# Kernel tuning notes

Hardware: AMD Instinct MI355X
Metric: run time of the kernel (lower is better)

## Reference

```python
import jax, jax.numpy as jnp
import numpy as np

B, T, H, NH, HD = 2, 2048, 2048, 16, 128


def setup_inputs() -> dict:
    key = jax.random.key(0)
    k1, k2, k3 = jax.random.split(key, 3)
    hidden_states = jax.random.normal(k1, (B, T, H), dtype=jnp.float32)
    w_qkv = jax.random.normal(k2, (3 * H, H), dtype=jnp.float32) * (1.0 / np.sqrt(H))
    w_out = jax.random.normal(k3, (H, H), dtype=jnp.float32) * (1.0 / np.sqrt(H))
    return {"hidden_states": hidden_states, "w_qkv": w_qkv, "w_out": w_out}


def reference(hidden_states, w_qkv, w_out):
    scale = 1.0 / np.sqrt(HD)
    # qkv projection: torch Linear is x @ W.T with W [out, in]
    qkv = jnp.einsum('bth,oh->bto', hidden_states, w_qkv)  # [B, T, 3H]
    q, k, v = jnp.split(qkv, 3, axis=2)
    # [B, NH, T, HD]
    q = q.reshape(B, T, NH, HD).transpose(0, 2, 1, 3)
    k = k.reshape(B, T, NH, HD).transpose(0, 2, 1, 3)
    v = v.reshape(B, T, NH, HD).transpose(0, 2, 1, 3)
    scores = jnp.einsum('bhqd,bhkd->bhqk', q, k) * scale  # [B, NH, T, T]
    mask = jnp.tril(jnp.ones((T, T), dtype=bool))  # causal
    scores = jnp.where(mask[None, None], scores, -jnp.inf)
    probs = jax.nn.softmax(scores, axis=-1)
    attn = jnp.einsum('bhqk,bhkd->bhqd', probs, v)  # [B, NH, T, HD]
    attn = attn.transpose(0, 2, 1, 3).reshape(B, T, H)
    out = jnp.einsum('bth,oh->bto', attn, w_out)
    return out
```

## Files before the change

kernel.cpp:

```cpp
#include <hip/hip_runtime.h>
#include <cstdint>
#include <cstddef>

typedef _Float16 f16x8 __attribute__((ext_vector_type(8)));
typedef _Float16 f16x4 __attribute__((ext_vector_type(4)));
typedef float    f32x4 __attribute__((ext_vector_type(4)));
typedef unsigned short ushort_t;

#define LOG2E 1.4426950408889634f

constexpr int BATCH = 2;
constexpr int TSEQ  = 2048;
constexpr int HID   = 2048;
constexpr int NH    = 16;
constexpr int HD    = 128;
constexpr int GK    = 2048;
constexpr int NKT   = GK / 64;

__device__ inline f32x4 mfma16(f16x8 a, f16x8 b, f32x4 c) {
    return __builtin_amdgcn_mfma_f32_16x16x32_f16(a, b, c, 0, 0, 0);
}

__device__ inline void async_copy16(const void* src, void* dst_lds) {
    __builtin_amdgcn_global_load_lds(
        (const __attribute__((address_space(1))) uint32_t*)src,
        (__attribute__((address_space(3))) uint32_t*)dst_lds, 16, 0, 0);
}

__global__ __launch_bounds__(256)
void cast_f32_f16(const float4* __restrict__ in, f16x4* __restrict__ out, int n4) {
    int i = blockIdx.x * 256 + threadIdx.x;
    if (i >= n4) return;
    float4 v = in[i];
    f16x4 o = { (_Float16)v.x, (_Float16)v.y, (_Float16)v.z, (_Float16)v.w };
    out[i] = o;
}

template <int MODE>
__global__ __launch_bounds__(512, 2)
void gemm_bt(const _Float16* __restrict__ A, const _Float16* __restrict__ B,
             float* __restrict__ C, _Float16* __restrict__ Qo,
             _Float16* __restrict__ Ko, _Float16* __restrict__ Vo, int NB) {
    __shared__ __align__(16) _Float16 As[3][256 * 64];
    __shared__ __align__(16) _Float16 Bs[3][128 * 64];

    const int tid  = threadIdx.x;
    const int lane = tid & 63;
    const int w    = tid >> 6;
    const int l15  = lane & 15;
    const int lq   = lane >> 4;
    const int wr   = w >> 1, wc = w & 1;

    const int bid = (int)blockIdx.x;
    const int cpx = (int)gridDim.x >> 3;
    const int swz = (bid & 7) * cpx + (bid >> 3);
    const int bn  = swz % NB, bm = swz / NB;
    const int m0  = bm * 256, n0 = bn * 128;

    const _Float16* Ab = A + (size_t)m0 * GK;
    const _Float16* Bb = B + (size_t)n0 * GK;

    auto stage = [&](int t, int b) {
        const int k0 = t * 64;
        #pragma unroll
        for (int it = 0; it < 4; ++it) {
            const int slot = it * 512 + tid;
            const int row = slot >> 3, c16 = slot & 7;
            const int srcb = c16 ^ (row & 7);
            async_copy16(Ab + (size_t)row * GK + k0 + srcb * 8,
                         (char*)As[b] + slot * 16);
        }
        #pragma unroll
        for (int it = 0; it < 2; ++it) {
            const int slot = it * 512 + tid;
            const int row = slot >> 3, c16 = slot & 7;
            const int srcb = c16 ^ (row & 7);
            async_copy16(Bb + (size_t)row * GK + k0 + srcb * 8,
                         (char*)Bs[b] + slot * 16);
        }
    };

    f32x4 acc[4][4] = {};

    stage(0, 0);
    stage(1, 1);

    for (int t = 0; t < NKT; ++t) {
        if (t + 1 < NKT) asm volatile("s_waitcnt vmcnt(6)" ::: "memory");
        else             asm volatile("s_waitcnt vmcnt(0)" ::: "memory");
        __builtin_amdgcn_s_barrier();
        __builtin_amdgcn_sched_barrier(0);

        const char* At_ = (const char*)As[t % 3];
        const char* Bt_ = (const char*)Bs[t % 3];

        f16x8 af[4][2], bff[4][2];
        #pragma unroll
        for (int i = 0; i < 4; ++i)
            #pragma unroll
            for (int kk = 0; kk < 2; ++kk) {
                const int ra = wr * 64 + i * 16 + l15;
                af[i][kk]  = *(const f16x8*)(At_ + ra * 128 + (((kk * 4 + lq) ^ (ra & 7)) << 4));
                const int rb = wc * 64 + i * 16 + l15;
                bff[i][kk] = *(const f16x8*)(Bt_ + rb * 128 + (((kk * 4 + lq) ^ (rb & 7)) << 4));
            }

        if (t + 2 < NKT) stage(t + 2, (t + 2) % 3);

        __builtin_amdgcn_s_setprio(1);
        #pragma unroll
        for (int kk = 0; kk < 2; ++kk)
            #pragma unroll
            for (int i = 0; i < 4; ++i)
                #pragma unroll
                for (int j = 0; j < 4; ++j)
                    acc[i][j] = mfma16(af[i][kk], bff[j][kk], acc[i][j]);
        __builtin_amdgcn_s_setprio(0);
    }

    if (MODE == 0) {
        #pragma unroll
        for (int j = 0; j < 4; ++j) {
            const int ncol = n0 + wc * 64 + j * 16 + l15;
            const int which = ncol >> 11;
            const int oo = ncol & 2047;
            const int head = oo >> 7;
            const int d = oo & 127;
            _Float16* dst = (which == 0) ? Qo : (which == 1) ? Ko : Vo;
            const float scl = (which == 0) ? 0.08838834764831845f : 1.0f;
            #pragma unroll
            for (int i = 0; i < 4; ++i) {
                #pragma unroll
                for (int r = 0; r < 4; ++r) {
                    const int m = m0 + wr * 64 + i * 16 + lq * 4 + r;
                    const int b = m >> 11, tt = m & 2047;
                    dst[((size_t)(b * NH + head) * TSEQ + tt) * HD + d] =
                        (_Float16)(acc[i][j][r] * scl);
                }
            }
        }
    } else {
        #pragma unroll
        for (int i = 0; i < 4; ++i)
            #pragma unroll
            for (int j = 0; j < 4; ++j)
                #pragma unroll
                for (int r = 0; r < 4; ++r) {
                    const int m = m0 + wr * 64 + i * 16 + lq * 4 + r;
                    const int n = n0 + wc * 64 + j * 16 + l15;
                    C[(size_t)m * HID + n] = acc[i][j][r];
                }
    }
}

__global__ __launch_bounds__(256)
void attn_fwd(const _Float16* __restrict__ Q, const _Float16* __restrict__ K,
              const _Float16* __restrict__ V, _Float16* __restrict__ O) {
    __shared__ __align__(16) char Ks[2][64 * 256];
    __shared__ __align__(16) char Vt[2][128 * 128];
    __shared__ __align__(16) char Ps[4][2048];

    const int tid  = threadIdx.x;
    const int lane = tid & 63;
    const int w    = tid >> 6;
    const int l15  = lane & 15;
    const int lq   = lane >> 4;

    const int bh   = (int)blockIdx.x & 31;
    const int pair = (int)blockIdx.x >> 5;
    const int b = bh >> 4, h = bh & 15;

    const size_t base = (size_t)bh * TSEQ * HD;
    const _Float16* Qp = Q + base;
    const _Float16* Kp = K + base;
    const _Float16* Vp = V + base;

    const f16x8 ones = { (_Float16)1.f, (_Float16)1.f, (_Float16)1.f, (_Float16)1.f,
                         (_Float16)1.f, (_Float16)1.f, (_Float16)1.f, (_Float16)1.f };

    uint4 vv[4];
    auto loadV = [&](int t) {
        const int row = tid & 63;
        #pragma unroll
        for (int it = 0; it < 4; ++it) {
            const int c8 = w * 4 + it;
            vv[it] = *(const uint4*)(Vp + (size_t)(t * 64 + row) * HD + c8 * 8);
        }
    };
    auto stageK = [&](int t, int buf) {
        #pragma unroll
        for (int it = 0; it < 4; ++it) {
            const int slot = it * 256 + tid;
            const int row = slot >> 4, c16 = slot & 15;
            const int srcb = c16 ^ (row & 7);
            async_copy16(Kp + (size_t)(t * 64 + row) * HD + srcb * 8, Ks[buf] + slot * 16);
        }
    };
    auto writeV = [&](int buf) {
        const int row = tid & 63;
        #pragma unroll
        for (int it = 0; it < 4; ++it) {
            const int c8 = w * 4 + it;
            const uint32_t wrd[4] = {vv[it].x, vv[it].y, vv[it].z, vv[it].w};
            #pragma unroll
            for (int p2 = 0; p2 < 4; ++p2) {
                const int d0 = c8 * 8 + p2 * 2, d1 = d0 + 1;
                int b0 = d0 * 128 + row * 2; b0 ^= (d0 & 7) << 4;
                int b1 = d1 * 128 + row * 2; b1 ^= (d1 & 7) << 4;
                *(ushort_t*)(Vt[buf] + b0) = (ushort_t)(wrd[p2] & 0xffffu);
                *(ushort_t*)(Vt[buf] + b1) = (ushort_t)(wrd[p2] >> 16);
            }
        }
    };

    char* Pb = Ps[w];

    for (int phase = 0; phase < 2; ++phase) {
        const int qt = phase ? pair : (31 - pair);
        const int q0 = qt * 64;
        const int NT = qt + 1;

        if (phase) __syncthreads();

        const int qrow = q0 + w * 16 + l15;
        f16x8 qf[4];
        #pragma unroll
        for (int ks = 0; ks < 4; ++ks)
            qf[ks] = *(const f16x8*)(Qp + (size_t)qrow * HD + ks * 32 + lq * 8);

        f32x4 o[8] = {};
        f32x4 osum = {};
        float m_run[4];
        #pragma unroll
        for (int r = 0; r < 4; ++r) m_run[r] = -1e30f;

        loadV(0);
        stageK(0, 0);

        int cur = 0;
        for (int t = 0; t < NT; ++t) {
            writeV(cur);
            __syncthreads();
            if (t + 1 < NT) {
                loadV(t + 1);
                stageK(t + 1, cur ^ 1);
            }

            const int kv0 = t * 64;
            f32x4 s[4] = {};
            __builtin_amdgcn_s_setprio(1);
            #pragma unroll
            for (int ks = 0; ks < 4; ++ks) {
                #pragma unroll
                for (int nf = 0; nf < 4; ++nf) {
                    const int r   = nf * 16 + l15;
                    const int blk = (ks * 4 + lq) ^ (r & 7);
                    const f16x8 kf = *(const f16x8*)(Ks[cur] + r * 256 + blk * 16);
                    s[nf] = mfma16(qf[ks], kf, s[nf]);
                }
            }
            __builtin_amdgcn_s_setprio(0);

            if (kv0 + 63 > q0 + w * 16) {
                #pragma unroll
                for (int nf = 0; nf < 4; ++nf) {
                    const int kvp = kv0 + nf * 16 + l15;
                    #pragma unroll
                    for (int r = 0; r < 4; ++r)
                        if (kvp > q0 + w * 16 + lq * 4 + r) s[nf][r] = -1e30f;
                }
            }

            bool need = false;
            #pragma unroll
            for (int r = 0; r < 4; ++r) {
                const float v = fmaxf(fmaxf(s[0][r], s[1][r]), fmaxf(s[2][r], s[3][r]));
                need = need || (v > m_run[r] + 5.0f);
            }
            if (__any(need)) {
                float alpha[4];
                #pragma unroll
                for (int r = 0; r < 4; ++r) {
                    float v = fmaxf(fmaxf(s[0][r], s[1][r]), fmaxf(s[2][r], s[3][r]));
                    v = fmaxf(v, __shfl_xor(v, 1));
                    v = fmaxf(v, __shfl_xor(v, 2));
                    v = fmaxf(v, __shfl_xor(v, 4));
                    v = fmaxf(v, __shfl_xor(v, 8));
                    const float mn = fmaxf(m_run[r], v);
                    alpha[r] = __builtin_exp2f((m_run[r] - mn) * LOG2E);
                    m_run[r] = mn;
                }
                #pragma unroll
                for (int df = 0; df < 8; ++df)
                    #pragma unroll
                    for (int r = 0; r < 4; ++r)
                        o[df][r] *= alpha[r];
                #pragma unroll
                for (int r = 0; r < 4; ++r) osum[r] *= alpha[r];
            }

            #pragma unroll
            for (int nf = 0; nf < 4; ++nf) {
                #pragma unroll
                for (int r = 0; r < 4; ++r) {
                    const float p = __builtin_exp2f((s[nf][r] - m_run[r]) * LOG2E);
                    const int qp = lq * 4 + r;
                    int byt = qp * 128 + (nf * 16 + l15) * 2;
                    byt ^= (qp & 7) << 4;
                    union { _Float16 hf; ushort_t u; } cv;
                    cv.hf = (_Float16)p;
                    *(ushort_t*)(Pb + byt) = cv.u;
                }
            }

            __builtin_amdgcn_s_setprio(1);
            #pragma unroll
            for (int ks2 = 0; ks2 < 2; ++ks2) {
                const int pblk = (ks2 * 4 + lq) ^ (l15 & 7);
                const f16x8 pf = *(const f16x8*)(Pb + l15 * 128 + pblk * 16);
                #pragma unroll
                for (int df = 0; df < 8; ++df) {
                    const int vr   = df * 16 + l15;
                    const int vblk = (ks2 * 4 + lq) ^ (vr & 7);
                    const f16x8 vf = *(const f16x8*)(Vt[cur] + vr * 128 + vblk * 16);
                    o[df] = mfma16(pf, vf, o[df]);
                }
                osum = mfma16(pf, ones, osum);
            }
            __builtin_amdgcn_s_setprio(0);
            cur ^= 1;
        }

        float rl[4];
        #pragma unroll
        for (int r = 0; r < 4; ++r) rl[r] = 1.0f / osum[r];
        #pragma unroll
        for (int df = 0; df < 8; ++df) {
            #pragma unroll
            for (int r = 0; r < 4; ++r) {
                const int qg = q0 + w * 16 + lq * 4 + r;
                const int dg = df * 16 + l15;
                O[((size_t)(b * TSEQ + qg)) * HID + h * HD + dg] =
                    (_Float16)(o[df][r] * rl[r]);
            }
        }
    }
}

extern "C" void kernel_launch(void* const* d_in, const int* in_sizes, int n_in,
                              void* d_out, int out_size, void* d_ws, size_t ws_size,
                              hipStream_t stream) {
    (void)in_sizes; (void)n_in; (void)out_size; (void)ws_size;
    const float* hs   = (const float*)d_in[0];
    const float* wqkv = (const float*)d_in[1];
    const float* wout = (const float*)d_in[2];

    char* ws = (char*)d_ws;
    size_t off = 0;
    _Float16* hs_h   = (_Float16*)(ws + off); off += (size_t)BATCH * TSEQ * HID * 2;
    _Float16* wqkv_h = (_Float16*)(ws + off); off += (size_t)3 * HID * HID * 2;
    _Float16* wout_h = (_Float16*)(ws + off); off += (size_t)HID * HID * 2;
    _Float16* Qh     = (_Float16*)(ws + off); off += (size_t)BATCH * NH * TSEQ * HD * 2;
    _Float16* Kh     = (_Float16*)(ws + off); off += (size_t)BATCH * NH * TSEQ * HD * 2;
    _Float16* Vh     = (_Float16*)(ws + off); off += (size_t)BATCH * NH * TSEQ * HD * 2;
    _Float16* At     = (_Float16*)(ws + off); off += (size_t)BATCH * TSEQ * HID * 2;

    const int n4_hs   = BATCH * TSEQ * HID / 4;
    const int n4_wqkv = 3 * HID * HID / 4;
    const int n4_wout = HID * HID / 4;
    cast_f32_f16<<<dim3((n4_hs   + 255) / 256), dim3(256), 0, stream>>>((const float4*)hs,   (f16x4*)hs_h,   n4_hs);
    cast_f32_f16<<<dim3((n4_wqkv + 255) / 256), dim3(256), 0, stream>>>((const float4*)wqkv, (f16x4*)wqkv_h, n4_wqkv);
    cast_f32_f16<<<dim3((n4_wout + 255) / 256), dim3(256), 0, stream>>>((const float4*)wout, (f16x4*)wout_h, n4_wout);

    gemm_bt<0><<<dim3(768), dim3(512), 0, stream>>>(
        hs_h, wqkv_h, nullptr, Qh, Kh, Vh, 48);

    attn_fwd<<<dim3(512), dim3(256), 0, stream>>>(Qh, Kh, Vh, At);

    gemm_bt<1><<<dim3(256), dim3(512), 0, stream>>>(
        At, wout_h, (float*)d_out, nullptr, nullptr, nullptr, 16);
}
```

Measured before the change: 274.1 us.

## Use 128-row query tiles per block with two 16-row sub-tiles per wave

The attention kernel no longer pairs two 64-row query tiles per block. Each block now handles one 128-row query tile, and each wave processes two 16-row query sub-tiles against every staged K/V tile. This reuses each K and V fragment loaded from LDS across twice as many MFMAs and halves the K/V global loads per query row. In exchange it doubles the accumulator registers (launch bounds set to 2 blocks per CU) and doubles the P scratch buffer. It also loses the causal load-balancing pairing, since blocks now have uneven work, launched largest-first.

```diff
diff --git a/kernel.cpp b/kernel.cpp
--- a/kernel.cpp
+++ b/kernel.cpp
@@ -153,12 +153,12 @@
     }
 }
 
-__global__ __launch_bounds__(256)
+__global__ __launch_bounds__(256, 2)
 void attn_fwd(const _Float16* __restrict__ Q, const _Float16* __restrict__ K,
               const _Float16* __restrict__ V, _Float16* __restrict__ O) {
     __shared__ __align__(16) char Ks[2][64 * 256];
     __shared__ __align__(16) char Vt[2][128 * 128];
-    __shared__ __align__(16) char Ps[4][2048];
+    __shared__ __align__(16) char Ps[4][4096];
 
     const int tid  = threadIdx.x;
     const int lane = tid & 63;
@@ -166,8 +166,8 @@
     const int l15  = lane & 15;
     const int lq   = lane >> 4;
 
-    const int bh   = (int)blockIdx.x & 31;
-    const int pair = (int)blockIdx.x >> 5;
+    const int qt = 15 - ((int)blockIdx.x >> 5);
+    const int bh = (int)blockIdx.x & 31;
     const int b = bh >> 4, h = bh & 15;
 
     const size_t base = (size_t)bh * TSEQ * HD;
@@ -175,8 +175,27 @@
     const _Float16* Kp = K + base;
     const _Float16* Vp = V + base;
 
+    const int q0 = qt * 128;
+    const int NT = 2 * qt + 2;
+    const int qw = q0 + w * 32;
+
     const f16x8 ones = { (_Float16)1.f, (_Float16)1.f, (_Float16)1.f, (_Float16)1.f,
                          (_Float16)1.f, (_Float16)1.f, (_Float16)1.f, (_Float16)1.f };
+
+    f16x8 qf[2][4];
+    #pragma unroll
+    for (int qh = 0; qh < 2; ++qh)
+        #pragma unroll
+        for (int ks = 0; ks < 4; ++ks)
+            qf[qh][ks] = *(const f16x8*)(Qp + (size_t)(qw + qh * 16 + l15) * HD + ks * 32 + lq * 8);
+
+    f32x4 o[8][2] = {};
+    f32x4 osum[2] = {};
+    float m_run[2][4];
+    #pragma unroll
+    for (int qh = 0; qh < 2; ++qh)
+        #pragma unroll
+        for (int r = 0; r < 4; ++r) m_run[qh][r] = -1e30f;
 
     uint4 vv[4];
     auto loadV = [&](int t) {
@@ -215,39 +234,21 @@
 
     char* Pb = Ps[w];
 
-    for (int phase = 0; phase < 2; ++phase) {
-        const int qt = phase ? pair : (31 - pair);
-        const int q0 = qt * 64;
-        const int NT = qt + 1;
-
-        if (phase) __syncthreads();
-
-        const int qrow = q0 + w * 16 + l15;
-        f16x8 qf[4];
-        #pragma unroll
-        for (int ks = 0; ks < 4; ++ks)
-            qf[ks] = *(const f16x8*)(Qp + (size_t)qrow * HD + ks * 32 + lq * 8);
-
-        f32x4 o[8] = {};
-        f32x4 osum = {};
-        float m_run[4];
-        #pragma unroll
-        for (int r = 0; r < 4; ++r) m_run[r] = -1e30f;
-
-        loadV(0);
-        stageK(0, 0);
-
-        int cur = 0;
-        for (int t = 0; t < NT; ++t) {
-            writeV(cur);
-            __syncthreads();
-            if (t + 1 < NT) {
-                loadV(t + 1);
-                stageK(t + 1, cur ^ 1);
-            }
-
-            const int kv0 = t * 64;
-            f32x4 s[4] = {};
+    loadV(0);
+    stageK(0, 0);
+
+    int cur = 0;
+    for (int t = 0; t < NT; ++t) {
+        writeV(cur);
+        __syncthreads();
+        if (t + 1 < NT) {
+            loadV(t + 1);
+            stageK(t + 1, cur ^ 1);
+        }
+
+        const int kv0 = t * 64;
+        if (kv0 <= qw + 31) {
+            f32x4 s[2][4] = {};
             __builtin_amdgcn_s_setprio(1);
             #pragma unroll
             for (int ks = 0; ks < 4; ++ks) {
@@ -256,95 +257,117 @@
                     const int r   = nf * 16 + l15;
                     const int blk = (ks * 4 + lq) ^ (r & 7);
                     const f16x8 kf = *(const f16x8*)(Ks[cur] + r * 256 + blk * 16);
-                    s[nf] = mfma16(qf[ks], kf, s[nf]);
+                    s[0][nf] = mfma16(qf[0][ks], kf, s[0][nf]);
+                    s[1][nf] = mfma16(qf[1][ks], kf, s[1][nf]);
                 }
             }
             __builtin_amdgcn_s_setprio(0);
 
-            if (kv0 + 63 > q0 + w * 16) {
-                #pragma unroll
-                for (int nf = 0; nf < 4; ++nf) {
-                    const int kvp = kv0 + nf * 16 + l15;
+            if (kv0 + 63 > qw) {
+                #pragma unroll
+                for (int qh = 0; qh < 2; ++qh)
+                    #pragma unroll
+                    for (int nf = 0; nf < 4; ++nf) {
+                        const int kvp = kv0 + nf * 16 + l15;
+                        #pragma unroll
+                        for (int r = 0; r < 4; ++r)
+                            if (kvp > qw + qh * 16 + lq * 4 + r) s[qh][nf][r] = -1e30f;
+                    }
+            }
+
+            float lmax[2][4];
+            bool need = false;
+            #pragma unroll
+            for (int qh = 0; qh < 2; ++qh)
+                #pragma unroll
+                for (int r = 0; r < 4; ++r) {
+                    const float v = fmaxf(fmaxf(s[qh][0][r], s[qh][1][r]),
+                                          fmaxf(s[qh][2][r], s[qh][3][r]));
+                    lmax[qh][r] = v;
+                    need = need || (v > m_run[qh][r] + 5.0f);
+                }
+            if (__any(need)) {
+                float alpha[2][4];
+                #pragma unroll
+                for (int qh = 0; qh < 2; ++qh)
+                    #pragma unroll
+                    for (int r = 0; r < 4; ++r) {
+                        float v = lmax[qh][r];
+                        v = fmaxf(v, __shfl_xor(v, 1));
+                        v = fmaxf(v, __shfl_xor(v, 2));
+                        v = fmaxf(v, __shfl_xor(v, 4));
+                        v = fmaxf(v, __shfl_xor(v, 8));
+                        const float mn = fmaxf(m_run[qh][r], v);
+                        alpha[qh][r] = __builtin_exp2f((m_run[qh][r] - mn) * LOG2E);
+                        m_run[qh][r] = mn;
+                    }
+                #pragma unroll
+                for (int df = 0; df < 8; ++df)
+                    #pragma unroll
+                    for (int qh = 0; qh < 2; ++qh)
+                        #pragma unroll
+                        for (int r = 0; r < 4; ++r)
+                            o[df][qh][r] *= alpha[qh][r];
+                #pragma unroll
+                for (int qh = 0; qh < 2; ++qh)
                     #pragma unroll
                     for (int r = 0; r < 4; ++r)
-                        if (kvp > q0 + w * 16 + lq * 4 + r) s[nf][r] = -1e30f;
-                }
-            }
-
-            bool need = false;
-            #pragma unroll
-            for (int r = 0; r < 4; ++r) {
-                const float v = fmaxf(fmaxf(s[0][r], s[1][r]), fmaxf(s[2][r], s[3][r]));
-                need = need || (v > m_run[r] + 5.0f);
-            }
-            if (__any(need)) {
-                float alpha[4];
-                #pragma unroll
-                for (int r = 0; r < 4; ++r) {
-                    float v = fmaxf(fmaxf(s[0][r], s[1][r]), fmaxf(s[2][r], s[3][r]));
-                    v = fmaxf(v, __shfl_xor(v, 1));
-                    v = fmaxf(v, __shfl_xor(v, 2));
-                    v = fmaxf(v, __shfl_xor(v, 4));
-                    v = fmaxf(v, __shfl_xor(v, 8));
-                    const float mn = fmaxf(m_run[r], v);
-                    alpha[r] = __builtin_exp2f((m_run[r] - mn) * LOG2E);
-                    m_run[r] = mn;
-                }
-                #pragma unroll
-                for (int df = 0; df < 8; ++df)
+                        osum[qh][r] *= alpha[qh][r];
+            }
+
+            #pragma unroll
+            for (int qh = 0; qh < 2; ++qh)
+                #pragma unroll
+                for (int nf = 0; nf < 4; ++nf)
                     #pragma unroll
-                    for (int r = 0; r < 4; ++r)
-                        o[df][r] *= alpha[r];
-                #pragma unroll
-                for (int r = 0; r < 4; ++r) osum[r] *= alpha[r];
-            }
-
-            #pragma unroll
-            for (int nf = 0; nf < 4; ++nf) {
-                #pragma unroll
-                for (int r = 0; r < 4; ++r) {
-                    const float p = __builtin_exp2f((s[nf][r] - m_run[r]) * LOG2E);
-                    const int qp = lq * 4 + r;
-                    int byt = qp * 128 + (nf * 16 + l15) * 2;
-                    byt ^= (qp & 7) << 4;
-                    union { _Float16 hf; ushort_t u; } cv;
-                    cv.hf = (_Float16)p;
-                    *(ushort_t*)(Pb + byt) = cv.u;
-                }
-            }
+                    for (int r = 0; r < 4; ++r) {
+                        const float p = __builtin_exp2f((s[qh][nf][r] - m_run[qh][r]) * LOG2E);
+                        const int qp = qh * 16 + lq * 4 + r;
+                        int byt = qp * 128 + (nf * 16 + l15) * 2;
+                        byt ^= (qp & 7) << 4;
+                        union { _Float16 hf; ushort_t u; } cv;
+                        cv.hf = (_Float16)p;
+                        *(ushort_t*)(Pb + byt) = cv.u;
+                    }
 
             __builtin_amdgcn_s_setprio(1);
             #pragma unroll
             for (int ks2 = 0; ks2 < 2; ++ks2) {
                 const int pblk = (ks2 * 4 + lq) ^ (l15 & 7);
-                const f16x8 pf = *(const f16x8*)(Pb + l15 * 128 + pblk * 16);
+                const f16x8 pf0 = *(const f16x8*)(Pb + l15 * 128 + pblk * 16);
+                const f16x8 pf1 = *(const f16x8*)(Pb + (16 + l15) * 128 + pblk * 16);
                 #pragma unroll
                 for (int df = 0; df < 8; ++df) {
                     const int vr   = df * 16 + l15;
                     const int vblk = (ks2 * 4 + lq) ^ (vr & 7);
                     const f16x8 vf = *(const f16x8*)(Vt[cur] + vr * 128 + vblk * 16);
-                    o[df] = mfma16(pf, vf, o[df]);
+                    o[df][0] = mfma16(pf0, vf, o[df][0]);
+                    o[df][1] = mfma16(pf1, vf, o[df][1]);
                 }
-                osum = mfma16(pf, ones, osum);
+                osum[0] = mfma16(pf0, ones, osum[0]);
+                osum[1] = mfma16(pf1, ones, osum[1]);
             }
             __builtin_amdgcn_s_setprio(0);
-            cur ^= 1;
-        }
-
-        float rl[4];
-        #pragma unroll
-        for (int r = 0; r < 4; ++r) rl[r] = 1.0f / osum[r];
-        #pragma unroll
-        for (int df = 0; df < 8; ++df) {
+        }
+        cur ^= 1;
+    }
+
+    float rl[2][4];
+    #pragma unroll
+    for (int qh = 0; qh < 2; ++qh)
+        #pragma unroll
+        for (int r = 0; r < 4; ++r) rl[qh][r] = 1.0f / osum[qh][r];
+    #pragma unroll
+    for (int df = 0; df < 8; ++df)
+        #pragma unroll
+        for (int qh = 0; qh < 2; ++qh)
             #pragma unroll
             for (int r = 0; r < 4; ++r) {
-                const int qg = q0 + w * 16 + lq * 4 + r;
+                const int qg = qw + qh * 16 + lq * 4 + r;
                 const int dg = df * 16 + l15;
                 O[((size_t)(b * TSEQ + qg)) * HID + h * HD + dg] =
-                    (_Float16)(o[df][r] * rl[r]);
-            }
-        }
-    }
+                    (_Float16)(o[df][qh][r] * rl[qh][r]);
+            }
 }
 
 extern "C" void kernel_launch(void* const* d_in, const int* in_sizes, int n_in,
```

Result: slower. 283.4 us (+3.4%).
